# Performance work log

Hardware: AMD Instinct MI355X
Metric: run time of the kernel (lower is better)

Reference implementation:

```python
import jax, jax.numpy as jnp
import numpy as np

IN_F = 256
OUT_F = 64
ALPHA = 0.2  # LeakyReLU negative slope
MASK_VAL = -9e15


def _glorot(key, shape):
    r = np.sqrt(6.0 / (shape[0] + shape[1]))
    return jax.random.uniform(key, shape, jnp.float32, -r, r)


def setup_inputs() -> dict:
    key = jax.random.key(0)
    k_h, k_adj, k_W, k_a = jax.random.split(key, 4)
    B, N = 4, 4096
    h = jax.random.normal(k_h, (B, N, IN_F), jnp.float32)
    adj = jax.random.randint(k_adj, (B, N, N), 0, 2, jnp.int32)
    W = _glorot(k_W, (IN_F, OUT_F))
    a = _glorot(k_a, (2 * OUT_F, 1))
    bias = jnp.zeros((OUT_F,), jnp.float32)
    return {"h": h, "adj": adj, "W": W, "a": a, "bias": bias}


def reference(h, adj, W, a, bias):
    # Wh: [B, N, F_out]
    Wh = jnp.matmul(h, W) + bias
    # additive attention: e_ij = leakyrelu(Wh_i . a1 + Wh_j . a2)
    Wh1 = jnp.matmul(Wh, a[:OUT_F, :])   # [B, N, 1]
    Wh2 = jnp.matmul(Wh, a[OUT_F:, :])   # [B, N, 1]
    e = Wh1 + jnp.swapaxes(Wh2, 2, 1)    # [B, N, N]
    e = jnp.where(e > 0, e, ALPHA * e)   # LeakyReLU
    e = jnp.where(adj > 0, e, MASK_VAL)
    attention = jax.nn.softmax(e, axis=2)
    h_prime = jnp.matmul(attention, Wh)  # [B, N, F_out]
    return jax.nn.elu(h_prime)           # concat=True -> ELU
```

## Files before the change

### kernel.cpp

```cpp
#include <hip/hip_runtime.h>
#include <hip/hip_bf16.h>
#include <cstdint>

#define IN_F 256
#define OUT_F 64
#define NB 4
#define NN 4096
#define ALPHA 0.2f

typedef __attribute__((ext_vector_type(4))) float f32x4;
typedef __attribute__((ext_vector_type(4))) int i32x4;
typedef __attribute__((ext_vector_type(8))) short bf16x8;

static __device__ __forceinline__ ushort f2bf(float x) {
  uint32_t u = __float_as_uint(x);
  uint32_t r = (u + 0x7fffu + ((u >> 16) & 1u)) >> 16;
  return (ushort)r;
}

static __device__ __forceinline__ void gl16(const void* g, void* l) {
  __builtin_amdgcn_global_load_lds(
      (const __attribute__((address_space(1))) void*)g,
      (__attribute__((address_space(3))) void*)l, 16, 0, 0);
}

__global__ __launch_bounds__(256) void k1_gemm(
    const float* __restrict__ h, const float* __restrict__ W,
    const float* __restrict__ a, const float* __restrict__ bias,
    ushort* __restrict__ WhT, float* __restrict__ Wh1, float* __restrict__ Wh2)
{
  __shared__ float hs[32][33];
  __shared__ float Ws[32][64];
  const int t  = threadIdx.x;
  const int tx = t & 15;
  const int ty = t >> 4;
  const int row0 = blockIdx.x * 32;

  float acc[2][4] = {};

  for (int k0 = 0; k0 < IN_F; k0 += 32) {
    {
      int r = t >> 3, c4 = t & 7;
      *(f32x4*)&hs[r][c4 * 4] =
          *(const f32x4*)(h + (size_t)(row0 + r) * IN_F + k0 + c4 * 4);
    }
    #pragma unroll
    for (int s = 0; s < 2; ++s) {
      int f4 = t + 256 * s;
      int kk = f4 >> 4, c4 = f4 & 15;
      *(f32x4*)&Ws[kk][c4 * 4] = *(const f32x4*)(W + (size_t)(k0 + kk) * OUT_F + c4 * 4);
    }
    __syncthreads();
    #pragma unroll 8
    for (int kk = 0; kk < 32; ++kk) {
      f32x4 bv = *(const f32x4*)&Ws[kk][tx * 4];
      float av0 = hs[ty * 2 + 0][kk];
      float av1 = hs[ty * 2 + 1][kk];
      #pragma unroll
      for (int j = 0; j < 4; ++j) {
        acc[0][j] += av0 * bv[j];
        acc[1][j] += av1 * bv[j];
      }
    }
    __syncthreads();
  }

  #pragma unroll
  for (int i = 0; i < 2; ++i) {
    int row = row0 + ty * 2 + i;
    float s1 = 0.f, s2 = 0.f;
    #pragma unroll
    for (int j = 0; j < 4; ++j) {
      float v = acc[i][j] + bias[tx * 4 + j];
      acc[i][j] = v;
      s1 += v * a[tx * 4 + j];
      s2 += v * a[64 + tx * 4 + j];
    }
    #pragma unroll
    for (int off = 1; off < 16; off <<= 1) {
      s1 += __shfl_xor(s1, off);
      s2 += __shfl_xor(s2, off);
    }
    if (tx == 0) { Wh1[row] = s1; Wh2[row] = s2; }
    int bb = row >> 12;
    int n  = row & 4095;
    #pragma unroll
    for (int j = 0; j < 4; ++j) {
      WhT[(((size_t)(bb * OUT_F + tx * 4 + j)) << 12) + n] = f2bf(acc[i][j]);
    }
  }
}

#define BUFSZ 24576
#define NDEPTH 5
#define WH2_OFF 122880
#define LDS_TOTAL 139264
__global__ __launch_bounds__(512) void k2_attn(
    const int* __restrict__ adj, const ushort* __restrict__ WhT,
    const float* __restrict__ Wh1, const float* __restrict__ Wh2,
    float* __restrict__ out)
{
  extern __shared__ char smem[];
  const int t  = threadIdx.x;
  const int l  = t & 63;
  const int w  = t >> 6;
  const int rq = w >> 1;
  const int kq = w & 1;
  const int g  = l >> 4;
  const int lr = l & 15;
  const int b  = blockIdx.y;
  const int r0 = blockIdx.x << 6;

  const float LOG2E = 1.4426950408889634f;
  const int   rowl  = rq * 16 + lr;
  const float wh1 = Wh1[(b << 12) + r0 + rowl];
  asm volatile("" :: "v"(wh1));

  const int*    adjb = adj + ((size_t)b << 24) + ((size_t)r0 << 12);
  const ushort* whb  = WhT + ((size_t)(b * OUT_F) << 12);
  const int rowA = t >> 4,           mlA = (t & 15) ^ (rowA & 7);
  const int rowB = (t + 512) >> 4,   mlB = (t & 15) ^ (rowB & 7);
  const int fW   = t >> 3,           mlW = (t & 7) ^ (fW & 7);
  const int*    srcA = adjb + (size_t)rowA * 4096 + mlA * 4;
  const int*    srcB = adjb + (size_t)rowB * 4096 + mlB * 4;
  const ushort* srcW = whb + ((size_t)fW << 12) + mlW * 8;
  const int ldsA = t << 4, ldsB = (t + 512) << 4, ldsW = 16384 + (t << 4);

  auto STAGE = [&](int s) {
    char* base = smem + (s % NDEPTH) * BUFSZ;
    gl16(srcA + s * 64, base + ldsA);
    gl16(srcB + s * 64, base + ldsB);
    gl16(srcW + s * 64, base + ldsW);
  };

  f32x4 a0 = {0.f,0.f,0.f,0.f}, a1 = {0.f,0.f,0.f,0.f};
  f32x4 a2 = {0.f,0.f,0.f,0.f}, a3 = {0.f,0.f,0.f,0.f};
  f32x4 as = {0.f,0.f,0.f,0.f};
  bf16x8 ones;
  #pragma unroll
  for (int i = 0; i < 8; ++i) ones[i] = (short)0x3F80;

  const int swzA = (rowl & 7) << 4;
  const int swzW = (lr & 7) << 4;
  const int offA0 = (kq * 128 + g * 32) ^ swzA;
  const int offA1 = (kq * 128 + g * 32 + 16) ^ swzA;
  const int offW  = (kq * 64 + g * 16) ^ swzW;

  auto COMPUTE = [&](int s) {
    const char* base = smem + (s % NDEPTH) * BUFSZ;
    i32x4 ad0 = *(const i32x4*)(base + rowl * 256 + offA0);
    i32x4 ad1 = *(const i32x4*)(base + rowl * 256 + offA1);
    const char* wb = base + 16384;
    bf16x8 b0 = *(const bf16x8*)(wb + (lr     ) * 128 + offW);
    bf16x8 b1 = *(const bf16x8*)(wb + (lr + 16) * 128 + offW);
    bf16x8 b2 = *(const bf16x8*)(wb + (lr + 32) * 128 + offW);
    bf16x8 b3 = *(const bf16x8*)(wb + (lr + 48) * 128 + offW);
    const char* w2b = smem + WH2_OFF + (s << 8) + kq * 128 + g * 32;
    f32x4 w20 = *(const f32x4*)(w2b);
    f32x4 w21 = *(const f32x4*)(w2b + 16);

    float p[8];
    #pragma unroll
    for (int i = 0; i < 8; ++i) {
      float w2 = (i < 4) ? w20[i] : w21[i - 4];
      int   am = (i < 4) ? ad0[i] : ad1[i - 4];
      float s_ = wh1 + w2;
      float lk = fmaf(ALPHA, fminf(s_, 0.f), fmaxf(s_, 0.f));
      float pe = exp2f(lk * LOG2E);
      p[i] = (am > 0) ? pe : 0.0f;
    }
    union { bf16x8 v; uint32_t u[4]; } af;
    #pragma unroll
    for (int i = 0; i < 4; ++i)
      asm("v_cvt_pk_bf16_f32 %0, %1, %2" : "=v"(af.u[i]) : "v"(p[2*i]), "v"(p[2*i+1]));

    as = __builtin_amdgcn_mfma_f32_16x16x32_bf16(af.v, ones, as, 0, 0, 0);
    a0 = __builtin_amdgcn_mfma_f32_16x16x32_bf16(af.v, b0,   a0, 0, 0, 0);
    a1 = __builtin_amdgcn_mfma_f32_16x16x32_bf16(af.v, b1,   a1, 0, 0, 0);
    a2 = __builtin_amdgcn_mfma_f32_16x16x32_bf16(af.v, b2,   a2, 0, 0, 0);
    a3 = __builtin_amdgcn_mfma_f32_16x16x32_bf16(af.v, b3,   a3, 0, 0, 0);
  };

  {
    const float* w2src = Wh2 + (b << 12);
    gl16(w2src + (t << 2),         smem + WH2_OFF + (t << 4));
    gl16(w2src + ((t + 512) << 2), smem + WH2_OFF + ((t + 512) << 4));
  }
  STAGE(0);
  STAGE(1);
  STAGE(2);
  STAGE(3);

  for (int s = 0; s < 64; ++s) {
    if (s < 61)      asm volatile("s_waitcnt vmcnt(9)" ::: "memory");
    else if (s == 61) asm volatile("s_waitcnt vmcnt(6)" ::: "memory");
    else if (s == 62) asm volatile("s_waitcnt vmcnt(3)" ::: "memory");
    else              asm volatile("s_waitcnt vmcnt(0)" ::: "memory");
    __builtin_amdgcn_s_barrier();
    COMPUTE(s);
    if (s < 60) STAGE(s + 4);
  }

  __syncthreads();
  float* sacc = (float*)smem;
  float* ssum = (float*)(smem + 34816);
  #pragma unroll
  for (int r = 0; r < 4; ++r) {
    int rr = rq * 16 + g * 4 + r;
    float* dst = sacc + (kq * 64 + rr) * 68;
    dst[ 0 + lr] = a0[r];
    dst[16 + lr] = a1[r];
    dst[32 + lr] = a2[r];
    dst[48 + lr] = a3[r];
    if (lr == 0) ssum[kq * 64 + rr] = as[r];
  }
  __syncthreads();

  const int row = t >> 3;
  const int c0  = (t & 7) << 3;
  const float* p0 = sacc + row * 68;
  const float* p1 = sacc + (64 + row) * 68;
  float d = ssum[row] + ssum[64 + row];
  float inv = 1.0f / d;
  f32x4 o0, o1;
  #pragma unroll
  for (int j = 0; j < 4; ++j) {
    float x = (p0[c0 + j] + p1[c0 + j]) * inv;
    o0[j] = x > 0.f ? x : expm1f(x);
    float y = (p0[c0 + 4 + j] + p1[c0 + 4 + j]) * inv;
    o1[j] = y > 0.f ? y : expm1f(y);
  }
  size_t ob = ((size_t)((b << 12) + r0 + row) << 6) + c0;
  *(f32x4*)(out + ob)     = o0;
  *(f32x4*)(out + ob + 4) = o1;
}

extern "C" void kernel_launch(void* const* d_in, const int* in_sizes, int n_in,
                              void* d_out, int out_size, void* d_ws, size_t ws_size,
                              hipStream_t stream) {
  const float* h    = (const float*)d_in[0];
  const int*   adj  = (const int*)d_in[1];
  const float* W    = (const float*)d_in[2];
  const float* a    = (const float*)d_in[3];
  const float* bias = (const float*)d_in[4];
  float* out = (float*)d_out;

  char* ws = (char*)d_ws;
  ushort* WhT = (ushort*)ws;
  float*  Wh1 = (float*)(ws + (size_t)NB * OUT_F * NN * 2);
  float*  Wh2 = Wh1 + NB * NN;

  (void)hipFuncSetAttribute((const void*)k2_attn,
                            hipFuncAttributeMaxDynamicSharedMemorySize, LDS_TOTAL);

  k1_gemm<<<dim3(NB * NN / 32), 256, 0, stream>>>(h, W, a, bias, WhT, Wh1, Wh2);
  k2_attn<<<dim3(NN / 64, NB), 512, LDS_TOTAL, stream>>>(adj, WhT, Wh1, Wh2, out);
}
```

Baseline: 74.94 us.

## Load Wh operands directly into registers and deepen adjacency LDS pipeline

The Wh (bf16) B-operands are now loaded straight from global memory into a 4-deep register ring instead of being staged through LDS. The LDS stage buffer shrinks to adjacency only, which allows a 6-deep pipeline, and launch bounds request 2 blocks per CU. LOG2E is folded into Wh1/Wh2 in the first kernel so the exp2 needs no extra multiply. The cost is more VGPR pressure and hand-tuned vmcnt counts that must match the exact order of loads issued.

```diff
diff --git a/kernel.cpp b/kernel.cpp
--- a/kernel.cpp
+++ b/kernel.cpp
@@ -7,6 +7,7 @@
 #define NB 4
 #define NN 4096
 #define ALPHA 0.2f
+#define LOG2E 1.4426950408889634f
 
 typedef __attribute__((ext_vector_type(4))) float f32x4;
 typedef __attribute__((ext_vector_type(4))) int i32x4;
@@ -23,6 +24,7 @@
       (const __attribute__((address_space(1))) void*)g,
       (__attribute__((address_space(3))) void*)l, 16, 0, 0);
 }
+#define FENCE() asm volatile("" ::: "memory")
 
 __global__ __launch_bounds__(256) void k1_gemm(
     const float* __restrict__ h, const float* __restrict__ W,
@@ -81,7 +83,7 @@
       s1 += __shfl_xor(s1, off);
       s2 += __shfl_xor(s2, off);
     }
-    if (tx == 0) { Wh1[row] = s1; Wh2[row] = s2; }
+    if (tx == 0) { Wh1[row] = s1 * LOG2E; Wh2[row] = s2 * LOG2E; }
     int bb = row >> 12;
     int n  = row & 4095;
     #pragma unroll
@@ -91,11 +93,11 @@
   }
 }
 
-#define BUFSZ 24576
-#define NDEPTH 5
-#define WH2_OFF 122880
-#define LDS_TOTAL 139264
-__global__ __launch_bounds__(512) void k2_attn(
+#define BUFSZ 16384
+#define NDEPTH 6
+#define WH2_OFF 98304
+#define LDS_TOTAL 114688
+__global__ __launch_bounds__(512, 2) void k2_attn(
     const int* __restrict__ adj, const ushort* __restrict__ WhT,
     const float* __restrict__ Wh1, const float* __restrict__ Wh2,
     float* __restrict__ out)
@@ -111,26 +113,31 @@
   const int b  = blockIdx.y;
   const int r0 = blockIdx.x << 6;
 
-  const float LOG2E = 1.4426950408889634f;
-  const int   rowl  = rq * 16 + lr;
-  const float wh1 = Wh1[(b << 12) + r0 + rowl];
+  const int   rowl = rq * 16 + lr;
+  const float wh1  = Wh1[(b << 12) + r0 + rowl];
   asm volatile("" :: "v"(wh1));
 
-  const int*    adjb = adj + ((size_t)b << 24) + ((size_t)r0 << 12);
-  const ushort* whb  = WhT + ((size_t)(b * OUT_F) << 12);
-  const int rowA = t >> 4,           mlA = (t & 15) ^ (rowA & 7);
-  const int rowB = (t + 512) >> 4,   mlB = (t & 15) ^ (rowB & 7);
-  const int fW   = t >> 3,           mlW = (t & 7) ^ (fW & 7);
-  const int*    srcA = adjb + (size_t)rowA * 4096 + mlA * 4;
-  const int*    srcB = adjb + (size_t)rowB * 4096 + mlB * 4;
-  const ushort* srcW = whb + ((size_t)fW << 12) + mlW * 8;
-  const int ldsA = t << 4, ldsB = (t + 512) << 4, ldsW = 16384 + (t << 4);
+  const int* adjb = adj + ((size_t)b << 24) + ((size_t)r0 << 12);
+  const int rowA = t >> 4,         mlA = (t & 15) ^ (rowA & 7);
+  const int rowB = (t + 512) >> 4, mlB = (t & 15) ^ (rowB & 7);
+  const int* srcA = adjb + (size_t)rowA * 4096 + mlA * 4;
+  const int* srcB = adjb + (size_t)rowB * 4096 + mlB * 4;
+  const int ldsA = t << 4, ldsB = 8192 + (t << 4);
 
   auto STAGE = [&](int s) {
     char* base = smem + (s % NDEPTH) * BUFSZ;
     gl16(srcA + s * 64, base + ldsA);
     gl16(srcB + s * 64, base + ldsB);
-    gl16(srcW + s * 64, base + ldsW);
+  };
+
+  const ushort* whb = WhT + ((size_t)(b * OUT_F + lr) << 12) + kq * 32 + g * 8;
+  bf16x8 bq[4][4];
+  auto BLOAD = [&](int s) {
+    const ushort* p = whb + s * 64;
+    bq[s & 3][0] = *(const bf16x8*)(p);
+    bq[s & 3][1] = *(const bf16x8*)(p + (16 << 12));
+    bq[s & 3][2] = *(const bf16x8*)(p + (32 << 12));
+    bq[s & 3][3] = *(const bf16x8*)(p + (48 << 12));
   };
 
   f32x4 a0 = {0.f,0.f,0.f,0.f}, a1 = {0.f,0.f,0.f,0.f};
@@ -140,21 +147,14 @@
   #pragma unroll
   for (int i = 0; i < 8; ++i) ones[i] = (short)0x3F80;
 
-  const int swzA = (rowl & 7) << 4;
-  const int swzW = (lr & 7) << 4;
+  const int swzA  = (rowl & 7) << 4;
   const int offA0 = (kq * 128 + g * 32) ^ swzA;
   const int offA1 = (kq * 128 + g * 32 + 16) ^ swzA;
-  const int offW  = (kq * 64 + g * 16) ^ swzW;
 
   auto COMPUTE = [&](int s) {
     const char* base = smem + (s % NDEPTH) * BUFSZ;
     i32x4 ad0 = *(const i32x4*)(base + rowl * 256 + offA0);
     i32x4 ad1 = *(const i32x4*)(base + rowl * 256 + offA1);
-    const char* wb = base + 16384;
-    bf16x8 b0 = *(const bf16x8*)(wb + (lr     ) * 128 + offW);
-    bf16x8 b1 = *(const bf16x8*)(wb + (lr + 16) * 128 + offW);
-    bf16x8 b2 = *(const bf16x8*)(wb + (lr + 32) * 128 + offW);
-    bf16x8 b3 = *(const bf16x8*)(wb + (lr + 48) * 128 + offW);
     const char* w2b = smem + WH2_OFF + (s << 8) + kq * 128 + g * 32;
     f32x4 w20 = *(const f32x4*)(w2b);
     f32x4 w21 = *(const f32x4*)(w2b + 16);
@@ -166,7 +166,7 @@
       int   am = (i < 4) ? ad0[i] : ad1[i - 4];
       float s_ = wh1 + w2;
       float lk = fmaf(ALPHA, fminf(s_, 0.f), fmaxf(s_, 0.f));
-      float pe = exp2f(lk * LOG2E);
+      float pe = exp2f(lk);
       p[i] = (am > 0) ? pe : 0.0f;
     }
     union { bf16x8 v; uint32_t u[4]; } af;
@@ -174,32 +174,53 @@
     for (int i = 0; i < 4; ++i)
       asm("v_cvt_pk_bf16_f32 %0, %1, %2" : "=v"(af.u[i]) : "v"(p[2*i]), "v"(p[2*i+1]));
 
-    as = __builtin_amdgcn_mfma_f32_16x16x32_bf16(af.v, ones, as, 0, 0, 0);
-    a0 = __builtin_amdgcn_mfma_f32_16x16x32_bf16(af.v, b0,   a0, 0, 0, 0);
-    a1 = __builtin_amdgcn_mfma_f32_16x16x32_bf16(af.v, b1,   a1, 0, 0, 0);
-    a2 = __builtin_amdgcn_mfma_f32_16x16x32_bf16(af.v, b2,   a2, 0, 0, 0);
-    a3 = __builtin_amdgcn_mfma_f32_16x16x32_bf16(af.v, b3,   a3, 0, 0, 0);
+    as = __builtin_amdgcn_mfma_f32_16x16x32_bf16(af.v, ones,        as, 0, 0, 0);
+    a0 = __builtin_amdgcn_mfma_f32_16x16x32_bf16(af.v, bq[s & 3][0], a0, 0, 0, 0);
+    a1 = __builtin_amdgcn_mfma_f32_16x16x32_bf16(af.v, bq[s & 3][1], a1, 0, 0, 0);
+    a2 = __builtin_amdgcn_mfma_f32_16x16x32_bf16(af.v, bq[s & 3][2], a2, 0, 0, 0);
+    a3 = __builtin_amdgcn_mfma_f32_16x16x32_bf16(af.v, bq[s & 3][3], a3, 0, 0, 0);
   };
 
+  BLOAD(0);  FENCE();
   {
     const float* w2src = Wh2 + (b << 12);
     gl16(w2src + (t << 2),         smem + WH2_OFF + (t << 4));
     gl16(w2src + ((t + 512) << 2), smem + WH2_OFF + ((t + 512) << 4));
   }
-  STAGE(0);
-  STAGE(1);
-  STAGE(2);
-  STAGE(3);
-
-  for (int s = 0; s < 64; ++s) {
-    if (s < 61)      asm volatile("s_waitcnt vmcnt(9)" ::: "memory");
-    else if (s == 61) asm volatile("s_waitcnt vmcnt(6)" ::: "memory");
-    else if (s == 62) asm volatile("s_waitcnt vmcnt(3)" ::: "memory");
-    else              asm volatile("s_waitcnt vmcnt(0)" ::: "memory");
-    __builtin_amdgcn_s_barrier();
-    COMPUTE(s);
-    if (s < 60) STAGE(s + 4);
-  }
+  FENCE();
+  STAGE(0);  FENCE();
+  BLOAD(1);  FENCE();
+  STAGE(1);  FENCE();
+  BLOAD(2);  FENCE();
+  STAGE(2);  STAGE(3);  STAGE(4);  FENCE();
+
+#define STEP(S, WAITOP, DO_B, DO_S)                     \
+  do {                                                  \
+    asm volatile(WAITOP ::: "memory");                  \
+    __builtin_amdgcn_s_barrier();                       \
+    COMPUTE(S);                                         \
+    FENCE();                                            \
+    if (DO_B) BLOAD((S) + 3);                           \
+    FENCE();                                            \
+    if (DO_S) STAGE((S) + 5);                           \
+    FENCE();                                            \
+  } while (0)
+
+  STEP(0, "s_waitcnt vmcnt(16)", 1, 1);
+  STEP(1, "s_waitcnt vmcnt(16)", 1, 1);
+  STEP(2, "s_waitcnt vmcnt(16)", 1, 1);
+
+  #pragma unroll 4
+  for (int s = 3; s < 59; ++s) {
+    STEP(s, "s_waitcnt vmcnt(14)", 1, 1);
+  }
+
+  STEP(59, "s_waitcnt vmcnt(14)", 1, 0);
+  STEP(60, "s_waitcnt vmcnt(12)", 1, 0);
+  STEP(61, "s_waitcnt vmcnt(10)", 0, 0);
+  STEP(62, "s_waitcnt vmcnt(4)",  0, 0);
+  STEP(63, "s_waitcnt vmcnt(0)",  0, 0);
+#undef STEP
 
   __syncthreads();
   float* sacc = (float*)smem;
```

Measured after the change: 95.37 us. 27.3% more time.

## Specialize waves for adj vs WhT async loads and fold log2e into Wh1/Wh2

Applied to the files above, without the earlier changes.

The staging of adjacency and WhT tiles is split by wave: waves 0-3 issue all adj global-to-LDS loads and waves 4-7 issue all WhT loads. Each has its own ring buffer and its own vmcnt wait thresholds, and the pipeline tail is unrolled. The LOG2E scaling is moved into k1, which removes one multiply per attention element in the hot loop. The kernel also gets launch_bounds(512,1). The kernel is likely near adjacency-bandwidth bound, so the gain from issuing loads differently may be limited. Per-wave wait counts add fragility.

```diff
diff --git a/kernel.cpp b/kernel.cpp
--- a/kernel.cpp
+++ b/kernel.cpp
@@ -7,6 +7,7 @@
 #define NB 4
 #define NN 4096
 #define ALPHA 0.2f
+#define LOG2E 1.4426950408889634f
 
 typedef __attribute__((ext_vector_type(4))) float f32x4;
 typedef __attribute__((ext_vector_type(4))) int i32x4;
@@ -23,6 +24,7 @@
       (const __attribute__((address_space(1))) void*)g,
       (__attribute__((address_space(3))) void*)l, 16, 0, 0);
 }
+#define FENCE() asm volatile("" ::: "memory")
 
 __global__ __launch_bounds__(256) void k1_gemm(
     const float* __restrict__ h, const float* __restrict__ W,
@@ -81,7 +83,7 @@
       s1 += __shfl_xor(s1, off);
       s2 += __shfl_xor(s2, off);
     }
-    if (tx == 0) { Wh1[row] = s1; Wh2[row] = s2; }
+    if (tx == 0) { Wh1[row] = s1 * LOG2E; Wh2[row] = s2 * LOG2E; }
     int bb = row >> 12;
     int n  = row & 4095;
     #pragma unroll
@@ -91,11 +93,13 @@
   }
 }
 
-#define BUFSZ 24576
 #define NDEPTH 5
+#define ADJ_BUF 16384
+#define WHT_OFF 81920
+#define WHT_BUF 8192
 #define WH2_OFF 122880
 #define LDS_TOTAL 139264
-__global__ __launch_bounds__(512) void k2_attn(
+__global__ __launch_bounds__(512, 1) void k2_attn(
     const int* __restrict__ adj, const ushort* __restrict__ WhT,
     const float* __restrict__ Wh1, const float* __restrict__ Wh2,
     float* __restrict__ out)
@@ -111,26 +115,44 @@
   const int b  = blockIdx.y;
   const int r0 = blockIdx.x << 6;
 
-  const float LOG2E = 1.4426950408889634f;
-  const int   rowl  = rq * 16 + lr;
-  const float wh1 = Wh1[(b << 12) + r0 + rowl];
+  const int   rowl = rq * 16 + lr;
+  const float wh1  = Wh1[(b << 12) + r0 + rowl];
   asm volatile("" :: "v"(wh1));
 
   const int*    adjb = adj + ((size_t)b << 24) + ((size_t)r0 << 12);
   const ushort* whb  = WhT + ((size_t)(b * OUT_F) << 12);
-  const int rowA = t >> 4,           mlA = (t & 15) ^ (rowA & 7);
-  const int rowB = (t + 512) >> 4,   mlB = (t & 15) ^ (rowB & 7);
-  const int fW   = t >> 3,           mlW = (t & 7) ^ (fW & 7);
-  const int*    srcA = adjb + (size_t)rowA * 4096 + mlA * 4;
-  const int*    srcB = adjb + (size_t)rowB * 4096 + mlB * 4;
-  const ushort* srcW = whb + ((size_t)fW << 12) + mlW * 8;
-  const int ldsA = t << 4, ldsB = (t + 512) << 4, ldsW = 16384 + (t << 4);
-
-  auto STAGE = [&](int s) {
-    char* base = smem + (s % NDEPTH) * BUFSZ;
-    gl16(srcA + s * 64, base + ldsA);
-    gl16(srcB + s * 64, base + ldsB);
-    gl16(srcW + s * 64, base + ldsW);
+
+  const int*    srcA[4]; int ldsA[4];
+  const ushort* srcW[2]; int ldsW[2];
+  if (w < 4) {
+    #pragma unroll
+    for (int i = 0; i < 4; ++i) {
+      int e   = ((w * 4 + i) << 6) + l;
+      int row = e >> 4;
+      int ch  = (e & 15) ^ (row & 7);
+      srcA[i] = adjb + (size_t)row * 4096 + (ch << 2);
+      ldsA[i] = e << 4;
+    }
+  } else {
+    #pragma unroll
+    for (int i = 0; i < 2; ++i) {
+      int e    = (((w - 4) * 2 + i) << 6) + l;
+      int feat = e >> 3;
+      int ch   = (e & 7) ^ (feat & 7);
+      srcW[i] = whb + ((size_t)feat << 12) + (ch << 3);
+      ldsW[i] = e << 4;
+    }
+  }
+
+  auto STAGE_A = [&](int s) {
+    char* base = smem + (s % NDEPTH) * ADJ_BUF;
+    #pragma unroll
+    for (int i = 0; i < 4; ++i) gl16(srcA[i] + (s << 6), base + ldsA[i]);
+  };
+  auto STAGE_W = [&](int s) {
+    char* base = smem + WHT_OFF + (s % NDEPTH) * WHT_BUF;
+    #pragma unroll
+    for (int i = 0; i < 2; ++i) gl16(srcW[i] + (s << 6), base + ldsW[i]);
   };
 
   f32x4 a0 = {0.f,0.f,0.f,0.f}, a1 = {0.f,0.f,0.f,0.f};
@@ -140,21 +162,20 @@
   #pragma unroll
   for (int i = 0; i < 8; ++i) ones[i] = (short)0x3F80;
 
-  const int swzA = (rowl & 7) << 4;
-  const int swzW = (lr & 7) << 4;
+  const int swzA  = (rowl & 7) << 4;
   const int offA0 = (kq * 128 + g * 32) ^ swzA;
   const int offA1 = (kq * 128 + g * 32 + 16) ^ swzA;
-  const int offW  = (kq * 64 + g * 16) ^ swzW;
+  const int offW  = (kq * 64 + g * 16) ^ ((lr & 7) << 4);
 
   auto COMPUTE = [&](int s) {
-    const char* base = smem + (s % NDEPTH) * BUFSZ;
-    i32x4 ad0 = *(const i32x4*)(base + rowl * 256 + offA0);
-    i32x4 ad1 = *(const i32x4*)(base + rowl * 256 + offA1);
-    const char* wb = base + 16384;
-    bf16x8 b0 = *(const bf16x8*)(wb + (lr     ) * 128 + offW);
-    bf16x8 b1 = *(const bf16x8*)(wb + (lr + 16) * 128 + offW);
-    bf16x8 b2 = *(const bf16x8*)(wb + (lr + 32) * 128 + offW);
-    bf16x8 b3 = *(const bf16x8*)(wb + (lr + 48) * 128 + offW);
+    const char* baseA = smem + (s % NDEPTH) * ADJ_BUF;
+    const char* baseW = smem + WHT_OFF + (s % NDEPTH) * WHT_BUF;
+    i32x4 ad0 = *(const i32x4*)(baseA + rowl * 256 + offA0);
+    i32x4 ad1 = *(const i32x4*)(baseA + rowl * 256 + offA1);
+    bf16x8 b0 = *(const bf16x8*)(baseW + (lr     ) * 128 + offW);
+    bf16x8 b1 = *(const bf16x8*)(baseW + (lr + 16) * 128 + offW);
+    bf16x8 b2 = *(const bf16x8*)(baseW + (lr + 32) * 128 + offW);
+    bf16x8 b3 = *(const bf16x8*)(baseW + (lr + 48) * 128 + offW);
     const char* w2b = smem + WH2_OFF + (s << 8) + kq * 128 + g * 32;
     f32x4 w20 = *(const f32x4*)(w2b);
     f32x4 w21 = *(const f32x4*)(w2b + 16);
@@ -166,7 +187,7 @@
       int   am = (i < 4) ? ad0[i] : ad1[i - 4];
       float s_ = wh1 + w2;
       float lk = fmaf(ALPHA, fminf(s_, 0.f), fmaxf(s_, 0.f));
-      float pe = exp2f(lk * LOG2E);
+      float pe = exp2f(lk);
       p[i] = (am > 0) ? pe : 0.0f;
     }
     union { bf16x8 v; uint32_t u[4]; } af;
@@ -184,22 +205,31 @@
   {
     const float* w2src = Wh2 + (b << 12);
     gl16(w2src + (t << 2),         smem + WH2_OFF + (t << 4));
-    gl16(w2src + ((t + 512) << 2), smem + WH2_OFF + ((t + 512) << 4));
-  }
-  STAGE(0);
-  STAGE(1);
-  STAGE(2);
-  STAGE(3);
-
-  for (int s = 0; s < 64; ++s) {
-    if (s < 61)      asm volatile("s_waitcnt vmcnt(9)" ::: "memory");
-    else if (s == 61) asm volatile("s_waitcnt vmcnt(6)" ::: "memory");
-    else if (s == 62) asm volatile("s_waitcnt vmcnt(3)" ::: "memory");
-    else              asm volatile("s_waitcnt vmcnt(0)" ::: "memory");
-    __builtin_amdgcn_s_barrier();
+    gl16(w2src + ((t + 512) << 2), smem + WH2_OFF + 8192 + (t << 4));
+  }
+  FENCE();
+  if (w < 4) { STAGE_A(0); STAGE_A(1); STAGE_A(2); STAGE_A(3); }
+  else       { STAGE_W(0); STAGE_W(1); STAGE_W(2); STAGE_W(3); }
+  FENCE();
+
+#define WAITB(NA, NW)                                                   \
+  do {                                                                  \
+    if (w < 4) asm volatile("s_waitcnt vmcnt(" #NA ")" ::: "memory");   \
+    else       asm volatile("s_waitcnt vmcnt(" #NW ")" ::: "memory");   \
+    __builtin_amdgcn_s_barrier();                                       \
+  } while (0)
+
+  for (int s = 0; s < 61; ++s) {
+    WAITB(12, 6);
     COMPUTE(s);
-    if (s < 60) STAGE(s + 4);
-  }
+    FENCE();
+    if (s < 60) { if (w < 4) STAGE_A(s + 4); else STAGE_W(s + 4); }
+    FENCE();
+  }
+  WAITB(8, 4);  COMPUTE(62 - 1);
+  WAITB(4, 2);  COMPUTE(62);
+  WAITB(0, 0);  COMPUTE(63);
+#undef WAITB
 
   __syncthreads();
   float* sacc = (float*)smem;
```

New measurement: 78.91 us. 5.3% more time.
